# Kernel tuning notes

Hardware: AMD Instinct MI355X
Metric: run time of the kernel (lower is better)

Reference implementation:

```python
import jax, jax.numpy as jnp
import numpy as np

D_MODEL = 1024
N_HEADS = 16
HEAD_DIM = D_MODEL // N_HEADS
D_FF = 4096
MAX_STEPS = 16
MAX_LEN = 64  # hardcoded in the module
LN_EPS = 1e-5


def _layer_norm(x, g, b):
    m = jnp.mean(x, axis=-1, keepdims=True)
    v = jnp.mean((x - m) ** 2, axis=-1, keepdims=True)
    return (x - m) * jax.lax.rsqrt(v + LN_EPS) * g + b


def setup_inputs() -> dict:
    key = jax.random.key(0)
    ks = jax.random.split(key, 12)
    B, S = 8, 1024
    std = 0.02
    return {
        "x": jax.random.normal(ks[0], (B, S, D_MODEL), dtype=jnp.float32),
        "step_embed": jax.random.normal(ks[1], (MAX_STEPS, D_MODEL), dtype=jnp.float32) * std,
        "qkv_w": jax.random.normal(ks[2], (D_MODEL, 3 * D_MODEL), dtype=jnp.float32) * std,
        "qkv_b": jnp.zeros((3 * D_MODEL,), dtype=jnp.float32),
        "out_w": jax.random.normal(ks[3], (D_MODEL, D_MODEL), dtype=jnp.float32) * std,
        "out_b": jnp.zeros((D_MODEL,), dtype=jnp.float32),
        "rel_pos_bias": jax.random.normal(ks[4], (2 * MAX_LEN - 1,), dtype=jnp.float32) * std,
        "w1": jax.random.normal(ks[5], (D_MODEL, D_FF), dtype=jnp.float32) * std,
        "b1": jnp.zeros((D_FF,), dtype=jnp.float32),
        "w2": jax.random.normal(ks[6], (D_FF, D_MODEL), dtype=jnp.float32) * std,
        "b2": jnp.zeros((D_MODEL,), dtype=jnp.float32),
        "ln1_g": jnp.ones((D_MODEL,), dtype=jnp.float32),
        "ln1_b": jnp.zeros((D_MODEL,), dtype=jnp.float32),
        "ln2_g": jnp.ones((D_MODEL,), dtype=jnp.float32),
        "ln2_b": jnp.zeros((D_MODEL,), dtype=jnp.float32),
        "think_step": 3,
    }


def reference(x, step_embed, qkv_w, qkv_b, out_w, out_b, rel_pos_bias,
              w1, b1, w2, b2, ln1_g, ln1_b, ln2_g, ln2_b, think_step):
    B, S, D = x.shape
    scale = HEAD_DIM ** -0.5

    # step embedding (clamped), broadcast over batch and sequence
    step = min(int(think_step), MAX_STEPS - 1)
    x = x + step_embed[step][None, None, :]

    # QKV projection -> (3, B, H, S, Dh)
    qkv = (x @ qkv_w + qkv_b).reshape(B, S, 3, N_HEADS, HEAD_DIM)
    qkv = jnp.transpose(qkv, (2, 0, 3, 1, 4))
    q, k, v = qkv[0], qkv[1], qkv[2]

    # attention scores with clamped relative-position bias
    scores = jnp.einsum("bhqd,bhkd->bhqk", q, k) * scale
    pos = jnp.arange(S)
    rel = jnp.clip(pos[:, None] - pos[None, :] + (MAX_LEN - 1), 0, 2 * MAX_LEN - 2)
    scores = scores + rel_pos_bias[rel][None, None, :, :]

    probs = jax.nn.softmax(scores, axis=-1)
    attn = jnp.einsum("bhqk,bhkd->bhqd", probs, v)
    attn = jnp.transpose(attn, (0, 2, 1, 3)).reshape(B, S, D)
    attn = attn @ out_w + out_b

    x = _layer_norm(x + attn, ln1_g, ln1_b)
    ffn = jax.nn.gelu(x @ w1 + b1, approximate=False) @ w2 + b2
    x = _layer_norm(x + ffn, ln2_g, ln2_b)
    return x
```

## Files before the change

### kernel.cpp

```cpp
#include <hip/hip_runtime.h>
#include <cstdint>
#include <cmath>

typedef unsigned short u16;
typedef unsigned int u32;
typedef __bf16 bf16x8 __attribute__((ext_vector_type(8)));
typedef float f32x4 __attribute__((ext_vector_type(4)));
typedef float f32x16 __attribute__((ext_vector_type(16)));

#define DEV __device__ __forceinline__

DEV u16 f2bf(float f) {
    union { float f; unsigned u; } a; a.f = f;
    unsigned u = a.u;
    return (u16)((u + 0x7FFFu + ((u >> 16) & 1u)) >> 16);
}

DEV float bf2f(u16 u) {
    union { u32 u; float f; } a; a.u = (u32)u << 16; return a.f;
}

DEV u32 pack2bf(float a, float b) {
    union { float f; u32 u; } ua, ub; ua.f = a; ub.f = b;
    return __builtin_amdgcn_perm(ub.u + 0x8000u, ua.u + 0x8000u, 0x07060302u);
}

DEV float fast_exp2(float x) {
    float r;
    asm("v_exp_f32 %0, %1" : "=v"(r) : "v"(x));
    return r;
}

DEV float fast_rcp(float x) {
    float r;
    asm("v_rcp_f32 %0, %1" : "=v"(r) : "v"(x));
    return r;
}

DEV float gelu_fast(float v) {
    float z = fabsf(v) * 0.70710678118f;
    float t = fast_rcp(1.f + 0.3275911f * z);
    float poly = ((((1.061405429f * t - 1.453152027f) * t + 1.421413741f) * t
                   - 0.284496736f) * t + 0.254829592f) * t;
    float e = fast_exp2(-z * z * 1.44269504088896f);
    float erfv = 1.f - poly * e;
    erfv = copysignf(erfv, v);
    return 0.5f * v * (1.f + erfv);
}

DEV void async16(void* lds, const void* g) {
    __builtin_amdgcn_global_load_lds(
        (const __attribute__((address_space(1))) unsigned int*)g,
        (__attribute__((address_space(3))) unsigned int*)lds, 16, 0, 0);
}

#define LOG2E 1.44269504088896f
#define PHI()   __builtin_amdgcn_s_setprio(1)
#define PLO()   __builtin_amdgcn_s_setprio(0)

__global__ __launch_bounds__(256)
void prep_k(const float* __restrict__ s0, u16* __restrict__ d0,
            const float* __restrict__ s1, u16* __restrict__ d1,
            const float* __restrict__ s2, u16* __restrict__ d2,
            const float* __restrict__ s3, u16* __restrict__ d3,
            const float* __restrict__ x, const float* __restrict__ se,
            const int* __restrict__ ts, u16* __restrict__ xb) {
    int b = blockIdx.x, tid = threadIdx.x;
    if (b < 12288) {
        __shared__ float tile[32][33];
        const float* src; u16* dst; int N, tidx;
        if (b < 3072)      { src = s0; dst = d0; N = 3072; tidx = b; }
        else if (b < 4096) { src = s1; dst = d1; N = 1024; tidx = b - 3072; }
        else if (b < 8192) { src = s2; dst = d2; N = 4096; tidx = b - 4096; }
        else               { src = s3; dst = d3; N = 1024; tidx = b - 8192; }
        int ntx = N >> 5;
        int n0 = (tidx % ntx) * 32, k0 = (tidx / ntx) * 32;
        int K = (b >= 8192) ? 4096 : 1024;
        int tx = tid & 31, ty = tid >> 5;
        #pragma unroll
        for (int i = ty; i < 32; i += 8) tile[i][tx] = src[(size_t)(k0 + i) * N + n0 + tx];
        __syncthreads();
        int jx = tid & 15, iy = tid >> 4;
        #pragma unroll
        for (int i = iy; i < 32; i += 16) {
            ushort2 u2;
            u2.x = f2bf(tile[2 * jx][i]);
            u2.y = f2bf(tile[2 * jx + 1][i]);
            *(ushort2*)&dst[(size_t)(n0 + i) * K + k0 + 2 * jx] = u2;
        }
    } else {
        int st = ts[0]; st = st < 0 ? 0 : (st > 15 ? 15 : st);
        size_t i = (size_t)(b - 12288) * 256 + tid;
        float4 v = ((const float4*)x)[i];
        int c = (int)(i & 255);
        float4 e = ((const float4*)(se + (size_t)st * 1024))[c];
        v.x += e.x; v.y += e.y; v.z += e.z; v.w += e.w;
        ushort4 u; u.x = f2bf(v.x); u.y = f2bf(v.y); u.z = f2bf(v.z); u.w = f2bf(v.w);
        ((ushort4*)xb)[i] = u;
    }
}

template<int EPI>
__global__ __launch_bounds__(256, 3)
void gemm_bt(const u16* __restrict__ A, const u16* __restrict__ Bt,
             const float* __restrict__ bias, int Kdim,
             u16* __restrict__ ob0, u16* __restrict__ ob1, u16* __restrict__ ob2,
             const u16* __restrict__ addb, float* __restrict__ outf,
             const float2* __restrict__ lnstats, const float* __restrict__ lng,
             const float* __restrict__ lnb) {
    __shared__ __align__(16) u16 lA[128 * 64];
    __shared__ __align__(16) u16 lB[128 * 64];
    const int tid = threadIdx.x, wave = tid >> 6, lane = tid & 63;
    const int m5 = lane & 31, h = lane >> 5;
    const int wm = wave >> 1, wn = wave & 1;
    const size_t m0 = (size_t)blockIdx.x * 128, n0 = (size_t)blockIdx.y * 128;
    const size_t kb = (size_t)Kdim * 2;

    f32x16 acc[2][2];
    #pragma unroll
    for (int i = 0; i < 2; i++)
        #pragma unroll
        for (int j = 0; j < 2; j++)
            #pragma unroll
            for (int e = 0; e < 16; e++) acc[i][j][e] = 0.f;

    const char* Ab = (const char*)A + m0 * kb;
    const char* Bb = (const char*)Bt + n0 * kb;

    auto stage = [&](const char* srcbase, u16* ldsb, int k0) {
        #pragma unroll
        for (int j = 0; j < 4; j++) {
            int loff = wave * 4096 + j * 1024 + lane * 16;
            int L = loff >> 4, r = L >> 3, c = L & 7, g = c ^ (r & 7);
            async16((char*)ldsb + loff, srcbase + (size_t)r * kb + (size_t)k0 * 2 + g * 16);
        }
    };

    stage(Ab, lA, 0); stage(Bb, lB, 0);
    const int r7 = m5 & 7;
    for (int k0 = 0; k0 < Kdim; k0 += 64) {
        __syncthreads();
        bf16x8 af[2][4], bfr[2][4];
        #pragma unroll
        for (int ti = 0; ti < 2; ti++) {
            int rowA = wm * 64 + ti * 32 + m5;
            int rowB = wn * 64 + ti * 32 + m5;
            #pragma unroll
            for (int kh = 0; kh < 4; kh++) {
                int cs = (kh * 2 + h) ^ r7;
                af[ti][kh]  = *(const bf16x8*)((const char*)lA + rowA * 128 + cs * 16);
                bfr[ti][kh] = *(const bf16x8*)((const char*)lB + rowB * 128 + cs * 16);
            }
        }
        __syncthreads();
        if (k0 + 64 < Kdim) { stage(Ab, lA, k0 + 64); stage(Bb, lB, k0 + 64); }
        #pragma unroll
        for (int kh = 0; kh < 4; kh++)
            #pragma unroll
            for (int ti = 0; ti < 2; ti++)
                #pragma unroll
                for (int tj = 0; tj < 2; tj++)
                    acc[ti][tj] = __builtin_amdgcn_mfma_f32_32x32x16_bf16(
                        af[ti][kh], bfr[tj][kh], acc[ti][tj], 0, 0, 0);
    }

    #pragma unroll
    for (int ti = 0; ti < 2; ti++) {
        #pragma unroll
        for (int tj = 0; tj < 2; tj++) {
            size_t col = n0 + wn * 64 + tj * 32 + m5;
            float bv = bias[col];
            if constexpr (EPI == 0) {
                size_t t = col >> 10, c = col & 1023, hh = c >> 6, dh = c & 63;
                #pragma unroll
                for (int g = 0; g < 4; g++) {
                    size_t row0 = m0 + wm * 64 + ti * 32 + 4 * h + 8 * g;
                    size_t bq = row0 >> 10, s0 = row0 & 1023;
                    if (t == 0) {
                        #pragma unroll
                        for (int r = 0; r < 4; r++)
                            ob0[((bq * 16 + hh) * 1024 + s0 + r) * 64 + dh] =
                                f2bf((acc[ti][tj][g * 4 + r] + bv) * 0.18033688011112f);
                    } else if (t == 1) {
                        #pragma unroll
                        for (int r = 0; r < 4; r++)
                            ob1[((bq * 16 + hh) * 1024 + s0 + r) * 64 + dh] =
                                f2bf(acc[ti][tj][g * 4 + r] + bv);
                    } else {
                        ushort4 tmp;
                        tmp.x = f2bf(acc[ti][tj][g * 4 + 0] + bv);
                        tmp.y = f2bf(acc[ti][tj][g * 4 + 1] + bv);
                        tmp.z = f2bf(acc[ti][tj][g * 4 + 2] + bv);
                        tmp.w = f2bf(acc[ti][tj][g * 4 + 3] + bv);
                        *(ushort4*)(ob2 + ((bq * 16 + hh) * 64 + dh) * 1024 + s0) = tmp;
                    }
                }
            } else if constexpr (EPI == 1) {
                #pragma unroll
                for (int g = 0; g < 4; g++)
                    #pragma unroll
                    for (int r = 0; r < 4; r++) {
                        size_t row = m0 + wm * 64 + ti * 32 + 4 * h + 8 * g + r;
                        float val = acc[ti][tj][g * 4 + r] + bv;
                        size_t o = row * 1024 + col;
                        ob0[o] = f2bf(bf2f(addb[o]) + val);
                    }
            } else if constexpr (EPI == 2) {
                #pragma unroll
                for (int g = 0; g < 4; g++)
                    #pragma unroll
                    for (int r = 0; r < 4; r++) {
                        size_t row = m0 + wm * 64 + ti * 32 + 4 * h + 8 * g + r;
                        float val = acc[ti][tj][g * 4 + r] + bv;
                        ob0[row * 4096 + col] = f2bf(gelu_fast(val));
                    }
            } else {
                float gv_ = lng[col], bv_ = lnb[col];
                #pragma unroll
                for (int g = 0; g < 4; g++)
                    #pragma unroll
                    for (int r = 0; r < 4; r++) {
                        size_t row = m0 + wm * 64 + ti * 32 + 4 * h + 8 * g + r;
                        float val = acc[ti][tj][g * 4 + r] + bv;
                        size_t o = row * 1024 + col;
                        float2 st = lnstats[row];
                        float yv = (bf2f(addb[o]) - st.x) * st.y * gv_ + bv_;
                        outf[o] = yv + val;
                    }
            }
        }
    }
}

__global__ __launch_bounds__(256, 2)
void attn_k(const u16* __restrict__ Q, const u16* __restrict__ K_, const u16* __restrict__ Vt,
            const float* __restrict__ relb, u16* __restrict__ Out) {
    __shared__ __align__(16) u16 sP[128 * 128];
    __shared__ __align__(16) u16 sK[128 * 64];
    __shared__ __align__(16) u16 sVt[64 * 128];
    __shared__ float sL[4][128];
    __shared__ float sLinv[128];
    __shared__ float sRel[128];

    const int tid = threadIdx.x, wave = tid >> 6, lane = tid & 63;
    const int m5 = lane & 31, h = lane >> 5;
    const int bid = blockIdx.x;
    const int swz = (bid & 7) * 128 + (bid >> 3);
    const int bh = swz >> 3, q0 = (swz & 7) * 128;
    const size_t base = (size_t)bh * 65536;

    if (tid < 127) sRel[tid] = relb[tid] * LOG2E;

    auto stageK = [&](int kv0) {
        const char* kbp = (const char*)(K_ + base + (size_t)kv0 * 64);
        #pragma unroll
        for (int j = 0; j < 4; j++) {
            int loff = wave * 4096 + j * 1024 + lane * 16;
            int L = loff >> 4, r = L >> 3, c = L & 7, g = c ^ (r & 7);
            async16((char*)sK + loff, kbp + (size_t)r * 128 + g * 16);
        }
    };
    auto stageV = [&](int kv0) {
        const char* vbp = (const char*)(Vt + base) + (size_t)kv0 * 2;
        #pragma unroll
        for (int j = 0; j < 4; j++) {
            int loff = wave * 4096 + j * 1024 + lane * 16;
            int L = loff >> 4, r = L >> 4, c = L & 15, g = c ^ (r & 15);
            async16((char*)sVt + loff, vbp + (size_t)r * 2048 + g * 16);
        }
    };

    {
        const char* qb = (const char*)(Q + base + (size_t)q0 * 64);
        #pragma unroll
        for (int j = 0; j < 4; j++) {
            int loff = wave * 4096 + j * 1024 + lane * 16;
            int L = loff >> 4, r = L >> 3, c = L & 7, g = c ^ (r & 7);
            async16((char*)sP + loff, qb + (size_t)r * 128 + g * 16);
        }
    }
    stageK(0); stageV(0);
    __syncthreads();

    bf16x8 qf[4][4];
    #pragma unroll
    for (int qt = 0; qt < 4; qt++) {
        int row = qt * 32 + m5;
        #pragma unroll
        for (int s = 0; s < 4; s++) {
            int cs = (2 * s + h) ^ (m5 & 7);
            qf[qt][s] = *(const bf16x8*)((const char*)sP + row * 128 + cs * 16);
        }
    }
    __syncthreads();

    const int qh = wave >> 1, dhh = wave & 1;
    f32x16 Oacc[2];
    #pragma unroll
    for (int i = 0; i < 2; i++)
        #pragma unroll
        for (int e = 0; e < 16; e++) Oacc[i][e] = 0.f;
    float lsum[4] = {0.f, 0.f, 0.f, 0.f};

    for (int t = 0; t < 8; t++) {
        const int kv0 = t * 128;
        const int kvr = wave * 32 + m5;
        bf16x8 kf[4];
        #pragma unroll
        for (int s = 0; s < 4; s++) {
            int cs = (2 * s + h) ^ (m5 & 7);
            kf[s] = *(const bf16x8*)((const char*)sK + kvr * 128 + cs * 16);
        }
        f32x16 sc[4];
        #pragma unroll
        for (int qt = 0; qt < 4; qt++)
            #pragma unroll
            for (int e = 0; e < 16; e++) sc[qt][e] = 0.f;
        PHI();
        #pragma unroll
        for (int s = 0; s < 4; s++)
            #pragma unroll
            for (int qt = 0; qt < 4; qt++)
                sc[qt] = __builtin_amdgcn_mfma_f32_32x32x16_bf16(kf[s], qf[qt][s], sc[qt], 0, 0, 0);
        PLO();

        const int kvb = kv0 + wave * 32 + 4 * h;
        const bool far_lo = (kv0 >= q0 + 190);
        const bool far_hi = (kv0 <= q0 - 190);
        #pragma unroll
        for (int qt = 0; qt < 4; qt++) {
            const int qs = q0 + qt * 32 + m5;
            if (far_lo || far_hi) {
                float cb = far_lo ? sRel[0] : sRel[126];
                #pragma unroll
                for (int e = 0; e < 16; e++) sc[qt][e] = fast_exp2(sc[qt][e] + cb);
            } else {
                int relbase = qs - kvb + 63;
                #pragma unroll
                for (int g = 0; g < 4; g++)
                    #pragma unroll
                    for (int r = 0; r < 4; r++) {
                        int rel = relbase - 8 * g - r;
                        rel = rel < 0 ? 0 : (rel > 126 ? 126 : rel);
                        sc[qt][4 * g + r] = fast_exp2(sc[qt][4 * g + r] + sRel[rel]);
                    }
            }
            #pragma unroll
            for (int e = 0; e < 16; e++) lsum[qt] += sc[qt][e];
            u32 pk[4][2];
            #pragma unroll
            for (int g = 0; g < 4; g++) {
                pk[g][0] = pack2bf(sc[qt][4 * g + 0], sc[qt][4 * g + 1]);
                pk[g][1] = pack2bf(sc[qt][4 * g + 2], sc[qt][4 * g + 3]);
            }
            const int q = qt * 32 + m5;
            char* prow = (char*)sP + q * 256;
            #pragma unroll
            for (int u = 0; u < 2; u++) {
                u32 s0 = h ? pk[2 * u][0] : pk[2 * u + 1][0];
                u32 s1 = h ? pk[2 * u][1] : pk[2 * u + 1][1];
                u32 r0 = __shfl_xor((int)s0, 32);
                u32 r1 = __shfl_xor((int)s1, 32);
                uint4 w;
                if (h == 0) { w.x = pk[2 * u][0]; w.y = pk[2 * u][1]; w.z = r0; w.w = r1; }
                else        { w.x = r0; w.y = r1; w.z = pk[2 * u + 1][0]; w.w = pk[2 * u + 1][1]; }
                int c16 = (4 * wave + 2 * u + h) ^ (q & 15);
                *(uint4*)(prow + c16 * 16) = w;
            }
        }
        __syncthreads();
        if (t < 7) stageK(kv0 + 128);

        #pragma unroll
        for (int s = 0; s < 8; s++) {
            int dh = dhh * 32 + m5;
            int cv = (2 * s + h) ^ (dh & 15);
            bf16x8 vf = *(const bf16x8*)((const char*)sVt + dh * 256 + cv * 16);
            #pragma unroll
            for (int qt = 0; qt < 2; qt++) {
                int q = qh * 64 + qt * 32 + m5;
                int cp = (2 * s + h) ^ (q & 15);
                bf16x8 pf = *(const bf16x8*)((const char*)sP + q * 256 + cp * 16);
                PHI();
                Oacc[qt] = __builtin_amdgcn_mfma_f32_32x32x16_bf16(pf, vf, Oacc[qt], 0, 0, 0);
                PLO();
            }
        }
        __syncthreads();
        if (t < 7) stageV(kv0 + 128);
    }

    #pragma unroll
    for (int qt = 0; qt < 4; qt++) lsum[qt] += __shfl_xor(lsum[qt], 32);
    if (h == 0) {
        #pragma unroll
        for (int qt = 0; qt < 4; qt++) sL[wave][qt * 32 + m5] = lsum[qt];
    }
    __syncthreads();
    if (tid < 128) sLinv[tid] = 1.f / (sL[0][tid] + sL[1][tid] + sL[2][tid] + sL[3][tid]);
    __syncthreads();

    const int b = bh >> 4, hh = bh & 15;
    const int dh = dhh * 32 + m5;
    #pragma unroll
    for (int qt = 0; qt < 2; qt++) {
        #pragma unroll
        for (int g = 0; g < 4; g++) {
            #pragma unroll
            for (int r = 0; r < 4; r++) {
                int rl = qh * 64 + qt * 32 + 4 * h + 8 * g + r;
                float val = Oacc[qt][4 * g + r] * sLinv[rl];
                size_t s = (size_t)(q0 + rl);
                Out[((size_t)b * 1024 + s) * 1024 + hh * 64 + dh] = f2bf(val);
            }
        }
    }
}

template<int MODE>
__global__ __launch_bounds__(256)
void ln_k(const float* __restrict__ in, const u16* __restrict__ inb,
          const float* __restrict__ g, const float* __restrict__ b,
          float* __restrict__ of, u16* __restrict__ ob, float2* __restrict__ stats) {
    __shared__ float ws1[4], ws2[4];
    int row = blockIdx.x, t = threadIdx.x;
    float4 v;
    if constexpr (MODE == 0) {
        v = ((const float4*)(in + (size_t)row * 1024))[t];
    } else {
        ushort4 uv = ((const ushort4*)(inb + (size_t)row * 1024))[t];
        v.x = bf2f(uv.x); v.y = bf2f(uv.y); v.z = bf2f(uv.z); v.w = bf2f(uv.w);
    }
    float s = v.x + v.y + v.z + v.w;
    float s2 = v.x * v.x + v.y * v.y + v.z * v.z + v.w * v.w;
    #pragma unroll
    for (int m = 1; m < 64; m <<= 1) { s += __shfl_xor(s, m); s2 += __shfl_xor(s2, m); }
    if ((t & 63) == 0) { ws1[t >> 6] = s; ws2[t >> 6] = s2; }
    __syncthreads();
    s = ws1[0] + ws1[1] + ws1[2] + ws1[3];
    s2 = ws2[0] + ws2[1] + ws2[2] + ws2[3];
    float mean = s * (1.f / 1024.f);
    float var = s2 * (1.f / 1024.f) - mean * mean;
    float inv = rsqrtf(var + 1e-5f);
    float4 gv = ((const float4*)g)[t], bv = ((const float4*)b)[t];
    float4 o;
    o.x = (v.x - mean) * inv * gv.x + bv.x;
    o.y = (v.y - mean) * inv * gv.y + bv.y;
    o.z = (v.z - mean) * inv * gv.z + bv.z;
    o.w = (v.w - mean) * inv * gv.w + bv.w;
    if constexpr (MODE == 0) {
        ((float4*)(of + (size_t)row * 1024))[t] = o;
    } else {
        ushort4 u; u.x = f2bf(o.x); u.y = f2bf(o.y); u.z = f2bf(o.z); u.w = f2bf(o.w);
        ((ushort4*)(ob + (size_t)row * 1024))[t] = u;
        if (t == 0) stats[row] = make_float2(mean, inv);
    }
}

extern "C" void kernel_launch(void* const* d_in, const int* in_sizes, int n_in,
                              void* d_out, int out_size, void* d_ws, size_t ws_size,
                              hipStream_t stream) {
    (void)in_sizes; (void)n_in; (void)out_size; (void)ws_size;
    const float* x          = (const float*)d_in[0];
    const float* step_embed = (const float*)d_in[1];
    const float* qkv_w      = (const float*)d_in[2];
    const float* qkv_b      = (const float*)d_in[3];
    const float* out_w      = (const float*)d_in[4];
    const float* out_b      = (const float*)d_in[5];
    const float* relb       = (const float*)d_in[6];
    const float* w1         = (const float*)d_in[7];
    const float* b1         = (const float*)d_in[8];
    const float* w2         = (const float*)d_in[9];
    const float* b2         = (const float*)d_in[10];
    const float* ln1g       = (const float*)d_in[11];
    const float* ln1b       = (const float*)d_in[12];
    const float* ln2g       = (const float*)d_in[13];
    const float* ln2b       = (const float*)d_in[14];
    const int*   tstep      = (const int*)d_in[15];
    float* out = (float*)d_out;

    char* p = (char*)d_ws;
    u16* wt_qkv = (u16*)p; p += (size_t)3072 * 1024 * 2;
    u16* wt_out = (u16*)p; p += (size_t)1024 * 1024 * 2;
    u16* wt_w1  = (u16*)p; p += (size_t)4096 * 1024 * 2;
    u16* wt_w2  = (u16*)p; p += (size_t)1024 * 4096 * 2;
    float2* lnstats = (float2*)p; p += (size_t)8192 * 8;
    u16* xseb   = (u16*)p; p += (size_t)8192 * 1024 * 2;
    u16* qbuf   = (u16*)p; p += (size_t)8192 * 1024 * 2;
    u16* kbuf   = (u16*)p; p += (size_t)8192 * 1024 * 2;
    u16* attnb  = (u16*)p; p += (size_t)8192 * 1024 * 2;
    p += (size_t)8192 * 1024 * 2;
    u16* res1b  = (u16*)p; p += (size_t)8192 * 1024 * 2;
    float* res2 = (float*)p; p += (size_t)8192 * 1024 * 4;
    u16*   y1b  = xseb;
    u16*   hbuf = qbuf;
    u16*   vtb  = res1b;

    prep_k<<<dim3(12288 + 8192), dim3(256), 0, stream>>>(qkv_w, wt_qkv, out_w, wt_out,
                                                         w1, wt_w1, w2, wt_w2,
                                                         x, step_embed, tstep, xseb);
    gemm_bt<0><<<dim3(64, 24), dim3(256), 0, stream>>>(xseb, wt_qkv, qkv_b, 1024,
                                                       qbuf, kbuf, vtb, (const u16*)nullptr, (float*)nullptr,
                                                       (const float2*)nullptr, (const float*)nullptr, (const float*)nullptr);
    attn_k<<<dim3(1024), dim3(256), 0, stream>>>(qbuf, kbuf, vtb, relb, attnb);
    gemm_bt<1><<<dim3(64, 8), dim3(256), 0, stream>>>(attnb, wt_out, out_b, 1024,
                                                      res1b, (u16*)nullptr, (u16*)nullptr, xseb, (float*)nullptr,
                                                      (const float2*)nullptr, (const float*)nullptr, (const float*)nullptr);
    ln_k<1><<<dim3(8192), dim3(256), 0, stream>>>((const float*)nullptr, res1b, ln1g, ln1b,
                                                  (float*)nullptr, y1b, lnstats);
    gemm_bt<2><<<dim3(64, 32), dim3(256), 0, stream>>>(y1b, wt_w1, b1, 1024,
                                                       hbuf, (u16*)nullptr, (u16*)nullptr, (const u16*)nullptr, (float*)nullptr,
                                                       (const float2*)nullptr, (const float*)nullptr, (const float*)nullptr);
    gemm_bt<3><<<dim3(64, 8), dim3(256), 0, stream>>>(hbuf, wt_w2, b2, 4096,
                                                      (u16*)nullptr, (u16*)nullptr, (u16*)nullptr, res1b, res2,
                                                      lnstats, ln1g, ln1b);
    ln_k<0><<<dim3(8192), dim3(256), 0, stream>>>(res2, (const u16*)nullptr, ln2g, ln2b,
                                                  out, (u16*)nullptr, (float2*)nullptr);
}
```

Baseline: 483.3 us.

## Split-K the FFN down-projection into two bf16 partials summed in final layernorm

The W2 GEMM (K=4096) is split into two K-halves across blockIdx.z, doubling the grid from 512 to 1024 blocks to improve occupancy across CUs. Each half writes a bf16 partial: the first holds bias plus the recomputed LN1 residual, the second only the raw accumulator. The final layernorm now reads and sums the two bf16 partials instead of one fp32 buffer. This adds an extra bf16 rounding of partial sums, which lowers accuracy, but the total bytes written and read stay about the same as before.

```diff
diff --git a/kernel.cpp b/kernel.cpp
--- a/kernel.cpp
+++ b/kernel.cpp
@@ -103,7 +103,7 @@
 template<int EPI>
 __global__ __launch_bounds__(256, 3)
 void gemm_bt(const u16* __restrict__ A, const u16* __restrict__ Bt,
-             const float* __restrict__ bias, int Kdim,
+             const float* __restrict__ bias, int Kdim, int Kstride,
              u16* __restrict__ ob0, u16* __restrict__ ob1, u16* __restrict__ ob2,
              const u16* __restrict__ addb, float* __restrict__ outf,
              const float2* __restrict__ lnstats, const float* __restrict__ lng,
@@ -114,7 +114,8 @@
     const int m5 = lane & 31, h = lane >> 5;
     const int wm = wave >> 1, wn = wave & 1;
     const size_t m0 = (size_t)blockIdx.x * 128, n0 = (size_t)blockIdx.y * 128;
-    const size_t kb = (size_t)Kdim * 2;
+    const size_t kb = (size_t)Kstride * 2;
+    const int koff = (EPI == 3) ? (int)blockIdx.z * Kdim : 0;
 
     f32x16 acc[2][2];
     #pragma unroll
@@ -124,8 +125,8 @@
             #pragma unroll
             for (int e = 0; e < 16; e++) acc[i][j][e] = 0.f;
 
-    const char* Ab = (const char*)A + m0 * kb;
-    const char* Bb = (const char*)Bt + n0 * kb;
+    const char* Ab = (const char*)A + m0 * kb + (size_t)koff * 2;
+    const char* Bb = (const char*)Bt + n0 * kb + (size_t)koff * 2;
 
     auto stage = [&](const char* srcbase, u16* ldsb, int k0) {
         #pragma unroll
@@ -215,18 +216,31 @@
                         ob0[row * 4096 + col] = f2bf(gelu_fast(val));
                     }
             } else {
-                float gv_ = lng[col], bv_ = lnb[col];
-                #pragma unroll
-                for (int g = 0; g < 4; g++)
+                u16* pb = ob0 + (size_t)blockIdx.z * (8192 * 1024);
+                if (blockIdx.z == 0) {
+                    float gv_ = lng[col], bv_ = lnb[col];
                     #pragma unroll
-                    for (int r = 0; r < 4; r++) {
-                        size_t row = m0 + wm * 64 + ti * 32 + 4 * h + 8 * g + r;
-                        float val = acc[ti][tj][g * 4 + r] + bv;
-                        size_t o = row * 1024 + col;
-                        float2 st = lnstats[row];
-                        float yv = (bf2f(addb[o]) - st.x) * st.y * gv_ + bv_;
-                        outf[o] = yv + val;
-                    }
+                    for (int g = 0; g < 4; g++)
+                        #pragma unroll
+                        for (int r = 0; r < 4; r++) {
+                            size_t row = m0 + wm * 64 + ti * 32 + 4 * h + 8 * g + r;
+                            float val = acc[ti][tj][g * 4 + r] + bv;
+                            size_t o = row * 1024 + col;
+                            float2 st = lnstats[row];
+                            float yv = (bf2f(addb[o]) - st.x) * st.y * gv_ + bv_;
+                            pb[o] = f2bf(yv + val);
+                        }
+                } else {
+                    #pragma unroll
+                    for (int g = 0; g < 4; g++)
+                        #pragma unroll
+                        for (int r = 0; r < 4; r++) {
+                            size_t row = m0 + wm * 64 + ti * 32 + 4 * h + 8 * g + r;
+                            float val = acc[ti][tj][g * 4 + r];
+                            size_t o = row * 1024 + col;
+                            pb[o] = f2bf(val);
+                        }
+                }
             }
         }
     }
@@ -419,17 +433,22 @@
 
 template<int MODE>
 __global__ __launch_bounds__(256)
-void ln_k(const float* __restrict__ in, const u16* __restrict__ inb,
+void ln_k(const u16* __restrict__ inb, const u16* __restrict__ inb2,
           const float* __restrict__ g, const float* __restrict__ b,
           float* __restrict__ of, u16* __restrict__ ob, float2* __restrict__ stats) {
     __shared__ float ws1[4], ws2[4];
     int row = blockIdx.x, t = threadIdx.x;
     float4 v;
-    if constexpr (MODE == 0) {
-        v = ((const float4*)(in + (size_t)row * 1024))[t];
-    } else {
+    if constexpr (MODE == 1) {
         ushort4 uv = ((const ushort4*)(inb + (size_t)row * 1024))[t];
         v.x = bf2f(uv.x); v.y = bf2f(uv.y); v.z = bf2f(uv.z); v.w = bf2f(uv.w);
+    } else {
+        ushort4 a4 = ((const ushort4*)(inb + (size_t)row * 1024))[t];
+        ushort4 b4 = ((const ushort4*)(inb2 + (size_t)row * 1024))[t];
+        v.x = bf2f(a4.x) + bf2f(b4.x);
+        v.y = bf2f(a4.y) + bf2f(b4.y);
+        v.z = bf2f(a4.z) + bf2f(b4.z);
+        v.w = bf2f(a4.w) + bf2f(b4.w);
     }
     float s = v.x + v.y + v.z + v.w;
     float s2 = v.x * v.x + v.y * v.y + v.z * v.z + v.w * v.w;
@@ -448,12 +467,12 @@
     o.y = (v.y - mean) * inv * gv.y + bv.y;
     o.z = (v.z - mean) * inv * gv.z + bv.z;
     o.w = (v.w - mean) * inv * gv.w + bv.w;
-    if constexpr (MODE == 0) {
-        ((float4*)(of + (size_t)row * 1024))[t] = o;
-    } else {
+    if constexpr (MODE == 1) {
         ushort4 u; u.x = f2bf(o.x); u.y = f2bf(o.y); u.z = f2bf(o.z); u.w = f2bf(o.w);
         ((ushort4*)(ob + (size_t)row * 1024))[t] = u;
         if (t == 0) stats[row] = make_float2(mean, inv);
+    } else {
+        ((float4*)(of + (size_t)row * 1024))[t] = o;
     }
 }
 
@@ -491,7 +510,7 @@
     u16* attnb  = (u16*)p; p += (size_t)8192 * 1024 * 2;
     p += (size_t)8192 * 1024 * 2;
     u16* res1b  = (u16*)p; p += (size_t)8192 * 1024 * 2;
-    float* res2 = (float*)p; p += (size_t)8192 * 1024 * 4;
+    u16* part   = (u16*)p; p += (size_t)8192 * 1024 * 2 * 2;
     u16*   y1b  = xseb;
     u16*   hbuf = qbuf;
     u16*   vtb  = res1b;
@@ -499,21 +518,21 @@
     prep_k<<<dim3(12288 + 8192), dim3(256), 0, stream>>>(qkv_w, wt_qkv, out_w, wt_out,
                                                          w1, wt_w1, w2, wt_w2,
                                                          x, step_embed, tstep, xseb);
-    gemm_bt<0><<<dim3(64, 24), dim3(256), 0, stream>>>(xseb, wt_qkv, qkv_b, 1024,
+    gemm_bt<0><<<dim3(64, 24), dim3(256), 0, stream>>>(xseb, wt_qkv, qkv_b, 1024, 1024,
                                                        qbuf, kbuf, vtb, (const u16*)nullptr, (float*)nullptr,
                                                        (const float2*)nullptr, (const float*)nullptr, (const float*)nullptr);
     attn_k<<<dim3(1024), dim3(256), 0, stream>>>(qbuf, kbuf, vtb, relb, attnb);
-    gemm_bt<1><<<dim3(64, 8), dim3(256), 0, stream>>>(attnb, wt_out, out_b, 1024,
+    gemm_bt<1><<<dim3(64, 8), dim3(256), 0, stream>>>(attnb, wt_out, out_b, 1024, 1024,
                                                       res1b, (u16*)nullptr, (u16*)nullptr, xseb, (float*)nullptr,
                                                       (const float2*)nullptr, (const float*)nullptr, (const float*)nullptr);
-    ln_k<1><<<dim3(8192), dim3(256), 0, stream>>>((const float*)nullptr, res1b, ln1g, ln1b,
+    ln_k<1><<<dim3(8192), dim3(256), 0, stream>>>(res1b, (const u16*)nullptr, ln1g, ln1b,
                                                   (float*)nullptr, y1b, lnstats);
-    gemm_bt<2><<<dim3(64, 32), dim3(256), 0, stream>>>(y1b, wt_w1, b1, 1024,
+    gemm_bt<2><<<dim3(64, 32), dim3(256), 0, stream>>>(y1b, wt_w1, b1, 1024, 1024,
                                                        hbuf, (u16*)nullptr, (u16*)nullptr, (const u16*)nullptr, (float*)nullptr,
                                                        (const float2*)nullptr, (const float*)nullptr, (const float*)nullptr);
-    gemm_bt<3><<<dim3(64, 8), dim3(256), 0, stream>>>(hbuf, wt_w2, b2, 4096,
-                                                      (u16*)nullptr, (u16*)nullptr, (u16*)nullptr, res1b, res2,
-                                                      lnstats, ln1g, ln1b);
-    ln_k<0><<<dim3(8192), dim3(256), 0, stream>>>(res2, (const u16*)nullptr, ln2g, ln2b,
+    gemm_bt<3><<<dim3(64, 8, 2), dim3(256), 0, stream>>>(hbuf, wt_w2, b2, 2048, 4096,
+                                                         part, (u16*)nullptr, (u16*)nullptr, res1b, (float*)nullptr,
+                                                         lnstats, ln1g, ln1b);
+    ln_k<2><<<dim3(8192), dim3(256), 0, stream>>>(part, part + (size_t)8192 * 1024, ln2g, ln2b,
                                                   out, (u16*)nullptr, (float2*)nullptr);
 }
```

Measured after the change: 521.1 us. +7.8%, slower.
